# Kernel tuning notes

Measured on AMD Instinct MI355X. Metric: run time of the kernel, lower is better.

Reference implementation:

```python
import jax, jax.numpy as jnp
import numpy as np

B, T, D, H = 1, 4096, 1024, 16
HD = D // H          # head_dim = 64
W_LOCAL = 256        # sliding-window half-width (hardcoded in module)
N_GLOBAL = 64        # number of global tokens (hardcoded in module)


def setup_inputs() -> dict:
    key = jax.random.key(0)
    ks = jax.random.split(key, 7)
    s = 0.02
    return {
        "hidden_states": jax.random.normal(ks[0], (B, T, D), dtype=jnp.float32),
        "Wqkv": jax.random.normal(ks[1], (D, 3 * D), dtype=jnp.float32) * s,
        "bqkv": jnp.zeros((3 * D,), dtype=jnp.float32),
        "Wout": jax.random.normal(ks[2], (D, D), dtype=jnp.float32) * s,
        "bout": jnp.zeros((D,), dtype=jnp.float32),
        "Wg": jax.random.normal(ks[3], (D, 1), dtype=jnp.float32) * s,
        "bg": jnp.zeros((1,), dtype=jnp.float32),
    }


def reference(hidden_states, Wqkv, bqkv, Wout, bout, Wg, bg):
    b, t, d = hidden_states.shape
    scale = 1.0 / jnp.sqrt(jnp.asarray(HD, hidden_states.dtype))

    qkv = hidden_states @ Wqkv + bqkv                     # [B,T,3D]
    q, k, v = jnp.split(qkv, 3, axis=-1)
    # [B,T,D] -> [B,H,T,HD]
    q, k, v = (x.reshape(b, t, H, HD).transpose(0, 2, 1, 3) for x in (q, k, v))

    # local sliding-window attention (dense scores masked to |i-j| <= w, as in source)
    idx = jnp.arange(t)
    local_mask = jnp.abs(idx[None, :] - idx[:, None]) <= W_LOCAL   # [T,T]
    scores = jnp.einsum('bhqd,bhkd->bhqk', q, k) * scale           # [B,H,T,T]
    scores = jnp.where(local_mask[None, None], scores, -jnp.inf)
    attn_local = jnp.einsum('bhqk,bhkd->bhqd', jax.nn.softmax(scores, axis=-1), v)

    # global-token attention: every query attends to the first N_GLOBAL tokens
    ng = min(N_GLOBAL, t)
    k_g = k[:, :, :ng, :]                                          # [B,H,G,HD]
    v_g = v[:, :, :ng, :]
    scores_g = jnp.einsum('bhqd,bhgd->bhqg', q, k_g) * scale       # [B,H,T,G]
    attn_global = jnp.einsum('bhqg,bhgd->bhqd', jax.nn.softmax(scores_g, axis=-1), v_g)

    # sigmoid gate combine, broadcast over heads and head_dim
    gate = jax.nn.sigmoid(hidden_states @ Wg + bg).reshape(b, 1, t, 1)
    out = (1.0 - gate) * attn_local + gate * attn_global           # [B,H,T,HD]
    out = out.transpose(0, 2, 1, 3).reshape(b, t, d)
    return out @ Wout + bout
```

## Files before the change

kernel.cpp:

```cpp
#include <hip/hip_runtime.h>

typedef _Float16 half8 __attribute__((ext_vector_type(8)));
typedef _Float16 half4_t __attribute__((ext_vector_type(4)));
typedef float f32x4 __attribute__((ext_vector_type(4)));

#define MFMA(a, b, c) __builtin_amdgcn_mfma_f32_16x16x32_f16(a, b, c, 0, 0, 0)

constexpr int T_TOK = 4096;
constexpr int DMODEL = 1024;
constexpr int WLOC = 256;

typedef const __attribute__((address_space(1))) uint32_t* gptr_t;
typedef __attribute__((address_space(3))) uint32_t* lptr_t;
static __device__ __forceinline__ void gl16(const void* g, void* l) {
  __builtin_amdgcn_global_load_lds((gptr_t)g, (lptr_t)l, 16, 0, 0);
}

__global__ __launch_bounds__(256) void k_castgate(const float* __restrict__ hs,
                                                  const float* __restrict__ Wg,
                                                  const float* __restrict__ bg,
                                                  _Float16* __restrict__ out,
                                                  float* __restrict__ gate) {
  int w = threadIdx.x >> 6, lane = threadIdx.x & 63;
  int t = blockIdx.x * 4 + w;
  const float* row = hs + (size_t)t * DMODEL;
  _Float16* orow = out + (size_t)t * DMODEL;
  float s = 0.f;
#pragma unroll
  for (int i = 0; i < 4; ++i) {
    int off = lane * 4 + i * 256;
    f32x4 v = *(const f32x4*)(row + off);
    f32x4 g = *(const f32x4*)(Wg + off);
    s += v[0] * g[0] + v[1] * g[1] + v[2] * g[2] + v[3] * g[3];
    half4_t h;
    h[0] = (_Float16)v[0]; h[1] = (_Float16)v[1];
    h[2] = (_Float16)v[2]; h[3] = (_Float16)v[3];
    *(half4_t*)(orow + off) = h;
  }
#pragma unroll
  for (int off = 32; off; off >>= 1) s += __shfl_xor(s, off);
  if (lane == 0) gate[t] = 1.f / (1.f + __expf(-(s + bg[0])));
}

__global__ __launch_bounds__(256) void k_transpose_cast(const float* __restrict__ in,
                                                        _Float16* __restrict__ out,
                                                        int R, int C) {
  __shared__ float tile[64][65];
  int r0 = blockIdx.y * 64, c0 = blockIdx.x * 64;
  int tr = threadIdx.x >> 4;
  int tc = (threadIdx.x & 15) * 4;
#pragma unroll
  for (int p = 0; p < 4; ++p) {
    int r = p * 16 + tr;
    f32x4 v = *(const f32x4*)&in[(size_t)(r0 + r) * C + c0 + tc];
    tile[r][tc + 0] = v[0]; tile[r][tc + 1] = v[1];
    tile[r][tc + 2] = v[2]; tile[r][tc + 3] = v[3];
  }
  __syncthreads();
#pragma unroll
  for (int p = 0; p < 4; ++p) {
    int c = p * 16 + tr;
    half4_t h;
    h[0] = (_Float16)tile[tc + 0][c];
    h[1] = (_Float16)tile[tc + 1][c];
    h[2] = (_Float16)tile[tc + 2][c];
    h[3] = (_Float16)tile[tc + 3][c];
    *(half4_t*)&out[(size_t)(c0 + c) * R + r0 + tc] = h;
  }
}

template <int MODE, int NBX>
__global__ __launch_bounds__(256) void k_gemm(const _Float16* __restrict__ A,
                                              const _Float16* __restrict__ Bt,
                                              const float* __restrict__ bias,
                                              float* __restrict__ Cout,
                                              _Float16* __restrict__ qh,
                                              _Float16* __restrict__ kh,
                                              _Float16* __restrict__ vt,
                                              int M, int N, int K) {
  __shared__ __align__(16) _Float16 As[2][128][32];
  __shared__ __align__(16) _Float16 Bs[2][128][32];
  int nwg = gridDim.x;
  int cpx = nwg >> 3;
  int orig = blockIdx.x;
  int wg = (orig & 7) * cpx + (orig >> 3);
  int bx = wg % NBX, by = wg / NBX;
  int m0 = by * 128, n0 = bx * 128;

  int tid = threadIdx.x;
  int lane = tid & 63, wave = tid >> 6;
  int wm = wave >> 1, wn = wave & 1;
  int lr = lane & 15, lk = (lane >> 4) * 8;
  int sr = tid >> 2, sc = (tid & 3) * 8;
  f32x4 acc[4][4] = {};

  auto stage = [&](int kt, int b) {
    gl16(&A[(size_t)(m0 + sr) * K + kt + sc],       &As[b][sr][sc]);
    gl16(&A[(size_t)(m0 + sr + 64) * K + kt + sc],  &As[b][sr + 64][sc]);
    gl16(&Bt[(size_t)(n0 + sr) * K + kt + sc],      &Bs[b][sr][sc]);
    gl16(&Bt[(size_t)(n0 + sr + 64) * K + kt + sc], &Bs[b][sr + 64][sc]);
  };

  stage(0, 0);
  __syncthreads();
  int cur = 0;
  for (int kt = 0; kt < K; kt += 32) {
    if (kt + 32 < K) stage(kt + 32, cur ^ 1);
    half8 af[4], bf[4];
#pragma unroll
    for (int i = 0; i < 4; ++i) af[i] = *(half8*)&As[cur][wm * 64 + i * 16 + lr][lk];
#pragma unroll
    for (int i = 0; i < 4; ++i) bf[i] = *(half8*)&Bs[cur][wn * 64 + i * 16 + lr][lk];
#pragma unroll
    for (int i = 0; i < 4; ++i)
#pragma unroll
      for (int j = 0; j < 4; ++j)
        acc[i][j] = MFMA(af[i], bf[j], acc[i][j]);
    __syncthreads();
    cur ^= 1;
  }

  int lg2 = lane >> 4;
#pragma unroll
  for (int j = 0; j < 4; ++j) {
    int n = n0 + wn * 64 + j * 16 + lr;
    float b = bias[n];
#pragma unroll
    for (int i = 0; i < 4; ++i) {
#pragma unroll
      for (int r = 0; r < 4; ++r) {
        int m = m0 + wm * 64 + i * 16 + lg2 * 4 + r;
        float v = acc[i][j][r] + b;
        if (MODE == 1) {
          Cout[(size_t)m * N + n] = v;
        } else {
          int hh = (n >> 6) & 15, d = n & 63;
          if (n < 1024)      qh[((size_t)hh * T_TOK + m) * 64 + d] = (_Float16)v;
          else if (n < 2048) kh[((size_t)hh * T_TOK + m) * 64 + d] = (_Float16)v;
          else               vt[((size_t)hh * 64 + d) * T_TOK + m] = (_Float16)v;
        }
      }
    }
  }
}

__global__ __launch_bounds__(256) void k_attn(const _Float16* __restrict__ q_all,
                                              const _Float16* __restrict__ k_all,
                                              const _Float16* __restrict__ vT_all,
                                              const float* __restrict__ gate,
                                              _Float16* __restrict__ attn_h) {
  __shared__ __align__(16) _Float16 Ks[64][72];
  __shared__ __align__(16) _Float16 Vs[64][72];
  __shared__ __align__(16) _Float16 P[4][16][72];

  int n = blockIdx.x;
  int o = (n & 7) * 128 + (n >> 3);
  int h = o >> 6, qb = o & 63;
  int q0 = qb * 64;
  int tid = threadIdx.x;
  int lane = tid & 63, w = tid >> 6;
  int lr = lane & 15, lgp = lane >> 4;

  const _Float16* qh = q_all + (size_t)h * T_TOK * 64;
  const _Float16* kh = k_all + (size_t)h * T_TOK * 64;
  const _Float16* vt = vT_all + (size_t)h * 64 * T_TOK;

  half8 aq0 = *(const half8*)&qh[(size_t)(q0 + w * 16 + lr) * 64 + lgp * 8];
  half8 aq1 = *(const half8*)&qh[(size_t)(q0 + w * 16 + lr) * 64 + 32 + lgp * 8];
#pragma unroll
  for (int j = 0; j < 8; ++j) { aq0[j] = aq0[j] * (_Float16)0.125f; aq1[j] = aq1[j] * (_Float16)0.125f; }

  int r8 = tid >> 3, c8 = (tid & 7) * 8;
  half8 kr0, kr1, vr0, vr1;

  auto ldregs = [&](int key0) {
    kr0 = *(const half8*)&kh[(size_t)(key0 + r8) * 64 + c8];
    kr1 = *(const half8*)&kh[(size_t)(key0 + r8 + 32) * 64 + c8];
    vr0 = *(const half8*)&vt[(size_t)r8 * T_TOK + key0 + c8];
    vr1 = *(const half8*)&vt[(size_t)(r8 + 32) * T_TOK + key0 + c8];
  };
  auto dswrite = [&]() {
    *(half8*)&Ks[r8][c8]      = kr0;
    *(half8*)&Ks[r8 + 32][c8] = kr1;
    *(half8*)&Vs[r8][c8]      = vr0;
    *(half8*)&Vs[r8 + 32][c8] = vr1;
  };

  f32x4 acc_g[4] = {}, acc_l[4] = {};
  float m_g = -1e30f, l_g = 0.f, m_l = -1e30f, l_l = 0.f;

  auto compute = [&](int key0, bool use_mask, f32x4 (&acc)[4], float& ms, float& ls) {
    f32x4 s[4] = {};
#pragma unroll
    for (int g = 0; g < 4; ++g) {
      half8 b0 = *(half8*)&Ks[g * 16 + lr][lgp * 8];
      half8 b1 = *(half8*)&Ks[g * 16 + lr][32 + lgp * 8];
      s[g] = MFMA(b0, aq0, s[g]);
      s[g] = MFMA(b1, aq1, s[g]);
    }
    if (use_mask) {
      int moff = key0 + lgp * 4 - (q0 + w * 16 + lr) + WLOC;
#pragma unroll
      for (int g = 0; g < 4; ++g)
#pragma unroll
        for (int r = 0; r < 4; ++r) {
          unsigned u = (unsigned)(moff + g * 16 + r);
          if (u > 2u * WLOC) s[g][r] = -1e30f;
        }
    }
    float mloc = -1e30f;
#pragma unroll
    for (int g = 0; g < 4; ++g)
#pragma unroll
      for (int r = 0; r < 4; ++r) mloc = fmaxf(mloc, s[g][r]);
    mloc = fmaxf(mloc, __shfl_xor(mloc, 16));
    mloc = fmaxf(mloc, __shfl_xor(mloc, 32));
    if (__any(mloc > ms)) {
      float mn = fmaxf(ms, mloc);
      float al = __expf(ms - mn);
      ms = mn;
      float alr[4];
#pragma unroll
      for (int r = 0; r < 4; ++r) alr[r] = __shfl(al, lgp * 4 + r);
#pragma unroll
      for (int dt = 0; dt < 4; ++dt)
#pragma unroll
        for (int r = 0; r < 4; ++r) acc[dt][r] *= alr[r];
      ls *= al;
    }
    float rsum = 0.f;
#pragma unroll
    for (int g = 0; g < 4; ++g)
#pragma unroll
      for (int r = 0; r < 4; ++r) {
        float p = __expf(s[g][r] - ms);
        s[g][r] = p;
        rsum += p;
      }
    rsum += __shfl_xor(rsum, 16);
    rsum += __shfl_xor(rsum, 32);
    ls += rsum;
#pragma unroll
    for (int g = 0; g < 4; ++g) {
      half4_t q4;
      q4[0] = (_Float16)s[g][0]; q4[1] = (_Float16)s[g][1];
      q4[2] = (_Float16)s[g][2]; q4[3] = (_Float16)s[g][3];
      *(half4_t*)&P[w][lr][g * 16 + lgp * 4] = q4;
    }
    half8 pa0 = *(half8*)&P[w][lr][lgp * 8];
    half8 pa1 = *(half8*)&P[w][lr][32 + lgp * 8];
#pragma unroll
    for (int dt = 0; dt < 4; ++dt) {
      half8 bv0 = *(half8*)&Vs[dt * 16 + lr][lgp * 8];
      half8 bv1 = *(half8*)&Vs[dt * 16 + lr][32 + lgp * 8];
      acc[dt] = MFMA(pa0, bv0, acc[dt]);
      acc[dt] = MFMA(pa1, bv1, acc[dt]);
    }
  };

  ldregs(0);
  dswrite();
  __syncthreads();
  int lo = q0 - WLOC; if (lo < 0) lo = 0;
  int hi = q0 + 63 + WLOC + 1; if (hi > T_TOK) hi = T_TOK;
  ldregs(lo);
  compute(0, false, acc_g, m_g, l_g);
  __syncthreads();
  dswrite();
  __syncthreads();

  for (int key0 = lo; key0 < hi; key0 += 64) {
    int nxt = key0 + 64;
    bool have_nxt = nxt < hi;
    if (have_nxt) ldregs(nxt);
    bool use_mask = (key0 < q0 - 192) || (key0 > q0 + 192);
    compute(key0, use_mask, acc_l, m_l, l_l);
    __syncthreads();
    if (have_nxt) { dswrite(); __syncthreads(); }
  }

  float llr[4], lgr[4];
#pragma unroll
  for (int r = 0; r < 4; ++r) {
    llr[r] = __shfl(l_l, lgp * 4 + r);
    lgr[r] = __shfl(l_g, lgp * 4 + r);
  }
#pragma unroll
  for (int r = 0; r < 4; ++r) {
    int q = q0 + w * 16 + lgp * 4 + r;
    float g = gate[q];
#pragma unroll
    for (int dt = 0; dt < 4; ++dt) {
      float o2 = (1.f - g) * (acc_l[dt][r] / llr[r]) + g * (acc_g[dt][r] / lgr[r]);
      attn_h[(size_t)q * DMODEL + h * 64 + dt * 16 + lr] = (_Float16)o2;
    }
  }
}

extern "C" void kernel_launch(void* const* d_in, const int* in_sizes, int n_in,
                              void* d_out, int out_size, void* d_ws, size_t ws_size,
                              hipStream_t stream) {
  const float* hs   = (const float*)d_in[0];
  const float* Wqkv = (const float*)d_in[1];
  const float* bqkv = (const float*)d_in[2];
  const float* Wout = (const float*)d_in[3];
  const float* bout = (const float*)d_in[4];
  const float* Wg   = (const float*)d_in[5];
  const float* bg   = (const float*)d_in[6];
  float* out = (float*)d_out;

  char* ws = (char*)d_ws;
  _Float16* hidden_h = (_Float16*)(ws);
  _Float16* Wqkv_t   = (_Float16*)(ws + 8388608);
  _Float16* Wout_t   = (_Float16*)(ws + 14680064);
  _Float16* q_h      = (_Float16*)(ws + 16777216);
  _Float16* k_h      = (_Float16*)(ws + 25165824);
  _Float16* vT_h     = (_Float16*)(ws + 33554432);
  float*    gate     = (float*)(ws + 41943040);
  _Float16* attn_h   = hidden_h;

  k_castgate<<<1024, 256, 0, stream>>>(hs, Wg, bg, hidden_h, gate);
  k_transpose_cast<<<dim3(48, 16), 256, 0, stream>>>(Wqkv, Wqkv_t, 1024, 3072);
  k_transpose_cast<<<dim3(16, 16), 256, 0, stream>>>(Wout, Wout_t, 1024, 1024);
  k_gemm<0, 24><<<768, 256, 0, stream>>>(hidden_h, Wqkv_t, bqkv, nullptr,
                                         q_h, k_h, vT_h, 4096, 3072, 1024);
  k_attn<<<1024, 256, 0, stream>>>(q_h, k_h, vT_h, gate, attn_h);
  k_gemm<1, 8><<<256, 256, 0, stream>>>(attn_h, Wout_t, bout, out,
                                        nullptr, nullptr, nullptr, 4096, 1024, 1024);
}
```

Before: 185.5 us.

## Triple-buffer GEMM K-loop with vmcnt waits and vectorize V-transpose stores

The GEMM main loop moves from double to triple buffering of LDS tiles. It issues loads two stages ahead and uses explicit s_waitcnt vmcnt plus a raw s_barrier in place of __syncthreads, so global-to-LDS loads overlap more with MFMA work. The epilogue also hoists the head/dim index math and packs the four transposed V values into a single half4 store. This raises LDS use per block from 32KB to 48KB, which may reduce occupancy, and correctness now depends on the hand-counted vmcnt values.

```diff
diff --git a/kernel.cpp b/kernel.cpp
--- a/kernel.cpp
+++ b/kernel.cpp
@@ -78,8 +78,8 @@
                                               _Float16* __restrict__ kh,
                                               _Float16* __restrict__ vt,
                                               int M, int N, int K) {
-  __shared__ __align__(16) _Float16 As[2][128][32];
-  __shared__ __align__(16) _Float16 Bs[2][128][32];
+  __shared__ __align__(16) _Float16 As[3][128][32];
+  __shared__ __align__(16) _Float16 Bs[3][128][32];
   int nwg = gridDim.x;
   int cpx = nwg >> 3;
   int orig = blockIdx.x;
@@ -101,23 +101,29 @@
     gl16(&Bt[(size_t)(n0 + sr + 64) * K + kt + sc], &Bs[b][sr + 64][sc]);
   };
 
+  int T = K >> 5;
   stage(0, 0);
-  __syncthreads();
-  int cur = 0;
-  for (int kt = 0; kt < K; kt += 32) {
-    if (kt + 32 < K) stage(kt + 32, cur ^ 1);
+  stage(32, 1);
+  asm volatile("s_waitcnt vmcnt(4)" ::: "memory");
+  __builtin_amdgcn_s_barrier();
+
+  for (int t = 0; t < T; ++t) {
+    int b = t % 3;
+    bool more = (t + 2 < T);
+    if (more) stage((t + 2) << 5, (t + 2) % 3);
     half8 af[4], bf[4];
 #pragma unroll
-    for (int i = 0; i < 4; ++i) af[i] = *(half8*)&As[cur][wm * 64 + i * 16 + lr][lk];
-#pragma unroll
-    for (int i = 0; i < 4; ++i) bf[i] = *(half8*)&Bs[cur][wn * 64 + i * 16 + lr][lk];
+    for (int i = 0; i < 4; ++i) af[i] = *(half8*)&As[b][wm * 64 + i * 16 + lr][lk];
+#pragma unroll
+    for (int i = 0; i < 4; ++i) bf[i] = *(half8*)&Bs[b][wn * 64 + i * 16 + lr][lk];
 #pragma unroll
     for (int i = 0; i < 4; ++i)
 #pragma unroll
       for (int j = 0; j < 4; ++j)
         acc[i][j] = MFMA(af[i], bf[j], acc[i][j]);
-    __syncthreads();
-    cur ^= 1;
+    if (more) asm volatile("s_waitcnt vmcnt(4)" ::: "memory");
+    else      asm volatile("s_waitcnt vmcnt(0)" ::: "memory");
+    __builtin_amdgcn_s_barrier();
   }
 
   int lg2 = lane >> 4;
@@ -127,17 +133,23 @@
     float b = bias[n];
 #pragma unroll
     for (int i = 0; i < 4; ++i) {
-#pragma unroll
-      for (int r = 0; r < 4; ++r) {
-        int m = m0 + wm * 64 + i * 16 + lg2 * 4 + r;
-        float v = acc[i][j][r] + b;
-        if (MODE == 1) {
-          Cout[(size_t)m * N + n] = v;
+      int mm0 = m0 + wm * 64 + i * 16 + lg2 * 4;
+      if (MODE == 1) {
+#pragma unroll
+        for (int r = 0; r < 4; ++r)
+          Cout[(size_t)(mm0 + r) * N + n] = acc[i][j][r] + b;
+      } else {
+        int hh = (n >> 6) & 15, d = n & 63;
+        if (n < 2048) {
+          _Float16* dst = (n < 1024) ? qh : kh;
+#pragma unroll
+          for (int r = 0; r < 4; ++r)
+            dst[((size_t)hh * T_TOK + mm0 + r) * 64 + d] = (_Float16)(acc[i][j][r] + b);
         } else {
-          int hh = (n >> 6) & 15, d = n & 63;
-          if (n < 1024)      qh[((size_t)hh * T_TOK + m) * 64 + d] = (_Float16)v;
-          else if (n < 2048) kh[((size_t)hh * T_TOK + m) * 64 + d] = (_Float16)v;
-          else               vt[((size_t)hh * 64 + d) * T_TOK + m] = (_Float16)v;
+          half4_t v4;
+#pragma unroll
+          for (int r = 0; r < 4; ++r) v4[r] = (_Float16)(acc[i][j][r] + b);
+          *(half4_t*)&vt[((size_t)hh * 64 + d) * T_TOK + mm0] = v4;
         }
       }
     }
```

After: 186.3 us. Within noise of the previous version (+0.4%).
